# Performance work log

Measured on AMD Instinct MI355X. Metric: run time of the kernel, lower is better.

## Reference

```python
import jax, jax.numpy as jnp
import numpy as np

VAR_EPS = 1e-05


def setup_inputs() -> dict:
    key = jax.random.key(0)
    k1, k2 = jax.random.split(key)
    B, T = 1024, 16384
    pred = jax.random.normal(k1, (B, T), dtype=jnp.float32)
    target = jax.random.normal(k2, (B, T), dtype=jnp.float32)
    return {"pred": pred, "target": target}


def reference(pred, target):
    # Per-row Pearson correlation, vectorized over the batch dimension.
    T = pred.shape[1]
    mp = jnp.mean(pred, axis=1, keepdims=True)
    mt = jnp.mean(target, axis=1, keepdims=True)
    cp = pred - mp                      # [B, T] centered
    ct = target - mt
    sp = jnp.sum(cp * cp, axis=1)       # [B] sum of squares
    st = jnp.sum(ct * ct, axis=1)
    num = jnp.sum(cp * ct, axis=1)      # [B] covariance numerator
    # torch.var uses unbiased estimator (correction=1)
    var_p = sp / (T - 1)
    var_t = st / (T - 1)
    denom = jnp.sqrt(sp * st)
    safe_denom = jnp.where(denom > 0, denom, 1.0)
    corr = num / safe_denom
    valid = (var_p > VAR_EPS) & (var_t > VAR_EPS) & (denom > 0) & ~jnp.isnan(corr)
    per_row = jnp.where(valid, 1.0 - corr, 1.0)
    return jnp.mean(per_row)
```

## Files before the change

kernel.cpp:

```cpp
#include <hip/hip_runtime.h>

#define T_LEN 16384
#define VAR_EPS 1e-5f

typedef float v4 __attribute__((ext_vector_type(4)));
#define NTL(P) __builtin_nontemporal_load(P)


#define ACC(P,Q)                                              \
    sp  += (P.x + P.y) + (P.z + P.w);                         \
    st  += (Q.x + Q.y) + (Q.z + Q.w);                         \
    spp += P.x*P.x + P.y*P.y + P.z*P.z + P.w*P.w;             \
    stt += Q.x*Q.x + Q.y*Q.y + Q.z*Q.z + Q.w*Q.w;             \
    spt += P.x*Q.x + P.y*Q.y + P.z*Q.z + P.w*Q.w;

__global__ __launch_bounds__(256) void pearson_half_kernel(
    const float* __restrict__ pred, const float* __restrict__ target,
    float* __restrict__ moments)
{
    const int blk  = blockIdx.x;
    const int row  = blk >> 1;
    const int half = blk & 1;
    const int tid  = threadIdx.x;

    const v4* __restrict__ p4 =
        (const v4*)(pred   + (size_t)row * T_LEN) + half * 2048;
    const v4* __restrict__ t4 =
        (const v4*)(target + (size_t)row * T_LEN) + half * 2048;

    float sp = 0.f, st = 0.f, spp = 0.f, stt = 0.f, spt = 0.f;

    v4 p0 = NTL(p4 + tid);        v4 t0 = NTL(t4 + tid);
    v4 p1 = NTL(p4 + tid + 256);  v4 t1 = NTL(t4 + tid + 256);
    v4 p2 = NTL(p4 + tid + 512);  v4 t2 = NTL(t4 + tid + 512);
    v4 p3 = NTL(p4 + tid + 768);  v4 t3 = NTL(t4 + tid + 768);

    ACC(p0, t0); p0 = NTL(p4 + tid + 1024); t0 = NTL(t4 + tid + 1024);
    ACC(p1, t1); p1 = NTL(p4 + tid + 1280); t1 = NTL(t4 + tid + 1280);
    ACC(p2, t2); p2 = NTL(p4 + tid + 1536); t2 = NTL(t4 + tid + 1536);
    ACC(p3, t3); p3 = NTL(p4 + tid + 1792); t3 = NTL(t4 + tid + 1792);
    ACC(p0, t0);
    ACC(p1, t1);
    ACC(p2, t2);
    ACC(p3, t3);

    #pragma unroll
    for (int off = 32; off > 0; off >>= 1) {
        sp  += __shfl_down(sp,  off);
        st  += __shfl_down(st,  off);
        spp += __shfl_down(spp, off);
        stt += __shfl_down(stt, off);
        spt += __shfl_down(spt, off);
    }

    __shared__ float ws[4][8];
    const int wid = tid >> 6;
    if ((tid & 63) == 0) {
        ws[wid][0] = sp;  ws[wid][1] = st;  ws[wid][2] = spp;
        ws[wid][3] = stt; ws[wid][4] = spt;
    }
    __syncthreads();

    if (tid == 0) {
        float* m = moments + (size_t)blk * 8;
        m[0] = ws[0][0] + ws[1][0] + ws[2][0] + ws[3][0];
        m[1] = ws[0][1] + ws[1][1] + ws[2][1] + ws[3][1];
        m[2] = ws[0][2] + ws[1][2] + ws[2][2] + ws[3][2];
        m[3] = ws[0][3] + ws[1][3] + ws[2][3] + ws[3][3];
        m[4] = ws[0][4] + ws[1][4] + ws[2][4] + ws[3][4];
    }
}

__global__ __launch_bounds__(1024) void pearson_final_kernel(
    const float* __restrict__ moments, float* __restrict__ out, int B)
{
    const int tid = threadIdx.x;
    float loss_sum = 0.f;

    for (int r = tid; r < B; r += 1024) {
        const float* m0 = moments + (size_t)r * 16;
        const float* m1 = m0 + 8;
        float S_p  = m0[0] + m1[0];
        float S_t  = m0[1] + m1[1];
        float S_pp = m0[2] + m1[2];
        float S_tt = m0[3] + m1[3];
        float S_pt = m0[4] + m1[4];

        const float T   = (float)T_LEN;
        const float inv = 1.0f / T;
        float cp2 = S_pp - S_p * S_p * inv;
        float ct2 = S_tt - S_t * S_t * inv;
        float num = S_pt - S_p * S_t * inv;

        float var_p = cp2 / (T - 1.0f);
        float var_t = ct2 / (T - 1.0f);
        float denom = sqrtf(cp2 * ct2);
        float safe  = (denom > 0.0f) ? denom : 1.0f;
        float corr  = num / safe;
        bool valid = (var_p > VAR_EPS) && (var_t > VAR_EPS) &&
                     (denom > 0.0f) && !isnan(corr);
        loss_sum += valid ? (1.0f - corr) : 1.0f;
    }

    #pragma unroll
    for (int off = 32; off > 0; off >>= 1)
        loss_sum += __shfl_down(loss_sum, off);

    __shared__ float ws[16];
    if ((tid & 63) == 0) ws[tid >> 6] = loss_sum;
    __syncthreads();

    if (tid == 0) {
        float tot = 0.f;
        #pragma unroll
        for (int w = 0; w < 16; ++w) tot += ws[w];
        out[0] = tot / (float)B;
    }
}

extern "C" void kernel_launch(void* const* d_in, const int* in_sizes, int n_in,
                              void* d_out, int out_size, void* d_ws, size_t ws_size,
                              hipStream_t stream) {
    const float* pred   = (const float*)d_in[0];
    const float* target = (const float*)d_in[1];
    float* out     = (float*)d_out;
    float* moments = (float*)d_ws;

    const int B = in_sizes[0] / T_LEN;

    pearson_half_kernel<<<B * 2, 256, 0, stream>>>(pred, target, moments);
    pearson_final_kernel<<<1, 1024, 0, stream>>>(moments, out, B);
}
```

Baseline: 138.7 us.

## Process one full row per block instead of splitting rows in halves

Each block now reduces an entire row of 16384 elements with a rolling four-deep load pipeline, instead of two blocks each reducing half a row. The grid shrinks from 2B to B blocks, and the final kernel reads one moment record per row with no pairwise combine. This cuts block count and partial writes but gives each block more serial work and fewer blocks to cover memory latency across the CUs.

```diff
diff --git a/kernel.cpp b/kernel.cpp
--- a/kernel.cpp
+++ b/kernel.cpp
@@ -14,35 +14,37 @@
     stt += Q.x*Q.x + Q.y*Q.y + Q.z*Q.z + Q.w*Q.w;             \
     spt += P.x*Q.x + P.y*Q.y + P.z*Q.z + P.w*Q.w;
 
-__global__ __launch_bounds__(256) void pearson_half_kernel(
+__global__ __launch_bounds__(256) void pearson_row_kernel(
     const float* __restrict__ pred, const float* __restrict__ target,
     float* __restrict__ moments)
 {
-    const int blk  = blockIdx.x;
-    const int row  = blk >> 1;
-    const int half = blk & 1;
-    const int tid  = threadIdx.x;
+    const int row = blockIdx.x;
+    const int tid = threadIdx.x;
 
-    const v4* __restrict__ p4 =
-        (const v4*)(pred   + (size_t)row * T_LEN) + half * 2048;
-    const v4* __restrict__ t4 =
-        (const v4*)(target + (size_t)row * T_LEN) + half * 2048;
+    const v4* __restrict__ p4 = (const v4*)(pred   + (size_t)row * T_LEN);
+    const v4* __restrict__ t4 = (const v4*)(target + (size_t)row * T_LEN);
 
     float sp = 0.f, st = 0.f, spp = 0.f, stt = 0.f, spt = 0.f;
 
-    v4 p0 = NTL(p4 + tid);        v4 t0 = NTL(t4 + tid);
-    v4 p1 = NTL(p4 + tid + 256);  v4 t1 = NTL(t4 + tid + 256);
-    v4 p2 = NTL(p4 + tid + 512);  v4 t2 = NTL(t4 + tid + 512);
-    v4 p3 = NTL(p4 + tid + 768);  v4 t3 = NTL(t4 + tid + 768);
+    v4 P[4], Q[4];
 
-    ACC(p0, t0); p0 = NTL(p4 + tid + 1024); t0 = NTL(t4 + tid + 1024);
-    ACC(p1, t1); p1 = NTL(p4 + tid + 1280); t1 = NTL(t4 + tid + 1280);
-    ACC(p2, t2); p2 = NTL(p4 + tid + 1536); t2 = NTL(t4 + tid + 1536);
-    ACC(p3, t3); p3 = NTL(p4 + tid + 1792); t3 = NTL(t4 + tid + 1792);
-    ACC(p0, t0);
-    ACC(p1, t1);
-    ACC(p2, t2);
-    ACC(p3, t3);
+    #pragma unroll
+    for (int s = 0; s < 4; ++s) {
+        P[s] = NTL(p4 + tid + 256 * s);
+        Q[s] = NTL(t4 + tid + 256 * s);
+    }
+
+    #pragma unroll
+    for (int i = 0; i < 12; ++i) {
+        ACC(P[i & 3], Q[i & 3]);
+        P[i & 3] = NTL(p4 + tid + 256 * (i + 4));
+        Q[i & 3] = NTL(t4 + tid + 256 * (i + 4));
+    }
+
+    #pragma unroll
+    for (int i = 12; i < 16; ++i) {
+        ACC(P[i & 3], Q[i & 3]);
+    }
 
     #pragma unroll
     for (int off = 32; off > 0; off >>= 1) {
@@ -62,7 +64,7 @@
     __syncthreads();
 
     if (tid == 0) {
-        float* m = moments + (size_t)blk * 8;
+        float* m = moments + (size_t)row * 8;
         m[0] = ws[0][0] + ws[1][0] + ws[2][0] + ws[3][0];
         m[1] = ws[0][1] + ws[1][1] + ws[2][1] + ws[3][1];
         m[2] = ws[0][2] + ws[1][2] + ws[2][2] + ws[3][2];
@@ -78,13 +80,12 @@
     float loss_sum = 0.f;
 
     for (int r = tid; r < B; r += 1024) {
-        const float* m0 = moments + (size_t)r * 16;
-        const float* m1 = m0 + 8;
-        float S_p  = m0[0] + m1[0];
-        float S_t  = m0[1] + m1[1];
-        float S_pp = m0[2] + m1[2];
-        float S_tt = m0[3] + m1[3];
-        float S_pt = m0[4] + m1[4];
+        const float* m = moments + (size_t)r * 8;
+        float S_p  = m[0];
+        float S_t  = m[1];
+        float S_pp = m[2];
+        float S_tt = m[3];
+        float S_pt = m[4];
 
         const float T   = (float)T_LEN;
         const float inv = 1.0f / T;
@@ -128,6 +129,6 @@
 
     const int B = in_sizes[0] / T_LEN;
 
-    pearson_half_kernel<<<B * 2, 256, 0, stream>>>(pred, target, moments);
+    pearson_row_kernel<<<B, 256, 0, stream>>>(pred, target, moments);
     pearson_final_kernel<<<1, 1024, 0, stream>>>(moments, out, B);
 }
```

After: 137.2 us. About the same (-1.1%).
